# Performance work log

Hardware: AMD Instinct MI355X
Metric: run time of the kernel (lower is better)

The kernel has to match this reference:

```python
import jax, jax.numpy as jnp
import numpy as np

N_INST = 2_000_000   # total instances
D_IN = 32
D_HID = 64
D_OUT = 1
NUM_BAGS = 100_000   # ids in [0, NUM_BAGS)


def setup_inputs() -> dict:
    key = jax.random.key(0)
    k0, k1, k2, k3, k4 = jax.random.split(key, 5)
    x = jax.random.normal(k0, (N_INST, D_IN), dtype=jnp.float32)
    # sorted bag ids, every bag present (contiguous bags of equal size -> a
    # valid instance of sorted_randint over [0, NUM_BAGS))
    ids = (jnp.arange(N_INST, dtype=jnp.int32) // (N_INST // NUM_BAGS))[None, :]
    W1 = jax.random.normal(k1, (D_IN, D_HID), dtype=jnp.float32) / np.sqrt(D_IN)
    b1 = jax.random.normal(k2, (D_HID,), dtype=jnp.float32) * 0.01
    W2 = jax.random.normal(k3, (D_HID, D_OUT), dtype=jnp.float32) / np.sqrt(D_HID)
    b2 = jax.random.normal(k4, (D_OUT,), dtype=jnp.float32) * 0.01
    return {"x": x, "ids": ids, "W1": W1, "b1": b1, "W2": W2, "b2": b2}


def reference(x, ids, W1, b1, W2, b2):
    inner_ids = ids[-1]                                    # [N] bag id per instance
    h = jax.nn.relu(x @ W1 + b1)                           # prepNN: [N, D_HID]
    # fused segment mean over bags (replaces the Python loop + boolean masks)
    sums = jax.ops.segment_sum(h, inner_ids, num_segments=NUM_BAGS)          # [B, D_HID]
    counts = jax.ops.segment_sum(jnp.ones((h.shape[0],), h.dtype), inner_ids,
                                 num_segments=NUM_BAGS)                      # [B]
    pooled = sums / counts[:, None]                        # aggregation_func = mean
    out = pooled @ W2 + b2                                 # afterNN: [B, D_OUT]
    return out
```

## Files before the change

kernel.cpp:

```cpp
#include <hip/hip_runtime.h>

#define NTHREADS 256

__global__ void __launch_bounds__(NTHREADS) bag_mlp_kernel(
    const float* __restrict__ x, const int* __restrict__ ids,
    const float* __restrict__ W1, const float* __restrict__ b1,
    const float* __restrict__ W2,
    float* __restrict__ bag_sum, float* __restrict__ bag_cnt, int n)
{
  const int lane = threadIdx.x & 63;
  const long i = (long)blockIdx.x * blockDim.x + threadIdx.x;
  const bool active = i < (long)n;

  float s = 0.f;
  float cnt = 0.f;
  int id = -1;

  if (active) {
    const float4* xp = (const float4*)(x + i * 32);
    float4 xr[8];
#pragma unroll
    for (int q = 0; q < 8; ++q) xr[q] = xp[q];
    const float* xv = (const float*)xr;

    id = ids[i];
    cnt = 1.f;

    float2 h[32];
    const float2* b1v = (const float2*)b1;
#pragma unroll
    for (int j = 0; j < 32; ++j) h[j] = b1v[j];

    const float2* W1v = (const float2*)W1;
#pragma unroll
    for (int k = 0; k < 32; ++k) {
      const float xk = xv[k];
#pragma unroll
      for (int j = 0; j < 32; ++j) {
        const float2 w = W1v[k * 32 + j];
        h[j].x = fmaf(xk, w.x, h[j].x);
        h[j].y = fmaf(xk, w.y, h[j].y);
      }
    }

    const float2* W2v = (const float2*)W2;
    float acc = 0.f;
#pragma unroll
    for (int j = 0; j < 32; ++j) {
      const float2 w = W2v[j];
      acc = fmaf(fmaxf(h[j].x, 0.f), w.x, acc);
      acc = fmaf(fmaxf(h[j].y, 0.f), w.y, acc);
    }
    s = acc;
  }

#pragma unroll
  for (int d = 1; d < 64; d <<= 1) {
    float s_up = __shfl_up(s, d, 64);
    float c_up = __shfl_up(cnt, d, 64);
    int   id_up = __shfl_up(id, d, 64);
    if (lane >= d && id_up == id) { s += s_up; cnt += c_up; }
  }
  const int id_dn = __shfl_down(id, 1, 64);
  const bool run_tail = (lane == 63) || (id != id_dn);
  if (run_tail && id >= 0) {
    atomicAdd(&bag_sum[id], s);
    atomicAdd(&bag_cnt[id], cnt);
  }
}

__global__ void __launch_bounds__(256) finalize_kernel(
    const float* __restrict__ bag_sum, const float* __restrict__ bag_cnt,
    const float* __restrict__ b2, float* __restrict__ out, int nbags)
{
  const int b = blockIdx.x * blockDim.x + threadIdx.x;
  if (b < nbags) out[b] = bag_sum[b] / bag_cnt[b] + b2[0];
}

extern "C" void kernel_launch(void* const* d_in, const int* in_sizes, int n_in,
                              void* d_out, int out_size, void* d_ws, size_t ws_size,
                              hipStream_t stream)
{
  const float* x  = (const float*)d_in[0];
  const int*   ids = (const int*)d_in[1];
  const float* W1 = (const float*)d_in[2];
  const float* b1 = (const float*)d_in[3];
  const float* W2 = (const float*)d_in[4];
  const float* b2 = (const float*)d_in[5];
  float* out = (float*)d_out;

  const int n     = in_sizes[0] / 32;
  const int nbags = out_size;

  float* bag_sum = (float*)d_ws;
  float* bag_cnt = bag_sum + nbags;

  hipMemsetAsync(d_ws, 0, (size_t)2 * nbags * sizeof(float), stream);

  const int blocks = (n + NTHREADS - 1) / NTHREADS;
  bag_mlp_kernel<<<blocks, NTHREADS, 0, stream>>>(x, ids, W1, b1, W2,
                                                  bag_sum, bag_cnt, n);

  finalize_kernel<<<(nbags + 255) / 256, 256, 0, stream>>>(bag_sum, bag_cnt,
                                                           b2, out, nbags);
}
```

Measured before the change: 419.1 us.

## Compute the hidden layer with bf16x3 MFMA over persistent 16-row wave tiles

Replaces the per-thread scalar FP32 MLP with MFMA 16x16x32 bf16 instructions. It emulates FP32 precision by splitting x and W1 into high and low bf16 parts and issuing three MFMAs per output tile. Each wave works through a contiguous range of 16-instance tiles on a fixed grid, prefetching the next tile. It merges same-bag partial sums before issuing atomics and drops the count buffer, recovering bag counts in finalize by binary search over the sorted ids. This cuts FP32 FMA work and atomic traffic, but it assumes n is a multiple of 16 and adds a small precision loss from the split bf16 products.

```diff
diff --git a/kernel.cpp b/kernel.cpp
--- a/kernel.cpp
+++ b/kernel.cpp
@@ -1,106 +1,162 @@
 #include <hip/hip_runtime.h>
 
-#define NTHREADS 256
+typedef __attribute__((ext_vector_type(8))) short short8v;
+typedef __attribute__((ext_vector_type(4))) float f32x4;
 
-__global__ void __launch_bounds__(NTHREADS) bag_mlp_kernel(
+__device__ __forceinline__ unsigned short f2bf(float f) {
+  unsigned u = __builtin_bit_cast(unsigned, f);
+  unsigned r = u + 0x7FFFu + ((u >> 16) & 1u);
+  return (unsigned short)(r >> 16);
+}
+__device__ __forceinline__ float bf2f(unsigned short h) {
+  unsigned u = ((unsigned)h) << 16;
+  return __builtin_bit_cast(float, u);
+}
+
+__global__ void __launch_bounds__(256) bag_mlp_mfma(
     const float* __restrict__ x, const int* __restrict__ ids,
     const float* __restrict__ W1, const float* __restrict__ b1,
     const float* __restrict__ W2,
-    float* __restrict__ bag_sum, float* __restrict__ bag_cnt, int n)
+    float* __restrict__ bag_sum, int ntiles, int tiles_per_wave)
 {
   const int lane = threadIdx.x & 63;
-  const long i = (long)blockIdx.x * blockDim.x + threadIdx.x;
-  const bool active = i < (long)n;
+  const int lm = lane & 15;
+  const int lg = lane >> 4;
+  const int wave = blockIdx.x * (blockDim.x >> 6) + (threadIdx.x >> 6);
 
-  float s = 0.f;
-  float cnt = 0.f;
-  int id = -1;
+  const int t0 = wave * tiles_per_wave;
+  const int t1 = min(t0 + tiles_per_wave, ntiles);
+  if (t0 >= t1) return;
 
-  if (active) {
-    const float4* xp = (const float4*)(x + i * 32);
-    float4 xr[8];
+  short8v bh[4], bl[4];
 #pragma unroll
-    for (int q = 0; q < 8; ++q) xr[q] = xp[q];
-    const float* xv = (const float*)xr;
+  for (int nt = 0; nt < 4; ++nt) {
+    const int col = lm + 16 * nt;
+#pragma unroll
+    for (int e = 0; e < 8; ++e) {
+      const int k = 16 * (e >> 2) + 4 * lg + (e & 3);
+      const float f = W1[k * 64 + col];
+      const unsigned short h = f2bf(f);
+      bh[nt][e] = (short)h;
+      bl[nt][e] = (short)f2bf(f - bf2f(h));
+    }
+  }
+  float b1c[4], w2c[4];
+#pragma unroll
+  for (int nt = 0; nt < 4; ++nt) {
+    b1c[nt] = b1[lm + 16 * nt];
+    w2c[nt] = W2[lm + 16 * nt];
+  }
 
-    id = ids[i];
-    cnt = 1.f;
+  float4 va, vb; int4 iv;
+  {
+    const long base = (long)t0 * 16;
+    const float* p = x + (base + lm) * 32 + 4 * lg;
+    va = *(const float4*)p;
+    vb = *(const float4*)(p + 16);
+    if (lm == 0) iv = *(const int4*)(ids + base + 4 * lg);
+  }
 
-    float2 h[32];
-    const float2* b1v = (const float2*)b1;
-#pragma unroll
-    for (int j = 0; j < 32; ++j) h[j] = b1v[j];
-
-    const float2* W1v = (const float2*)W1;
-#pragma unroll
-    for (int k = 0; k < 32; ++k) {
-      const float xk = xv[k];
-#pragma unroll
-      for (int j = 0; j < 32; ++j) {
-        const float2 w = W1v[k * 32 + j];
-        h[j].x = fmaf(xk, w.x, h[j].x);
-        h[j].y = fmaf(xk, w.y, h[j].y);
-      }
+  for (int t = t0; t < t1; ++t) {
+    float4 nva, nvb; int4 niv;
+    if (t + 1 < t1) {
+      const long base = (long)(t + 1) * 16;
+      const float* p = x + (base + lm) * 32 + 4 * lg;
+      nva = *(const float4*)p;
+      nvb = *(const float4*)(p + 16);
+      if (lm == 0) niv = *(const int4*)(ids + base + 4 * lg);
     }
 
-    const float2* W2v = (const float2*)W2;
-    float acc = 0.f;
+    short8v ah, al;
 #pragma unroll
-    for (int j = 0; j < 32; ++j) {
-      const float2 w = W2v[j];
-      acc = fmaf(fmaxf(h[j].x, 0.f), w.x, acc);
-      acc = fmaf(fmaxf(h[j].y, 0.f), w.y, acc);
+    for (int j = 0; j < 4; ++j) {
+      const float f = ((const float*)&va)[j];
+      const unsigned short h = f2bf(f);
+      ah[j] = (short)h; al[j] = (short)f2bf(f - bf2f(h));
+      const float g = ((const float*)&vb)[j];
+      const unsigned short h2 = f2bf(g);
+      ah[4 + j] = (short)h2; al[4 + j] = (short)f2bf(g - bf2f(h2));
     }
-    s = acc;
-  }
 
+    f32x4 acc[4];
 #pragma unroll
-  for (int d = 1; d < 64; d <<= 1) {
-    float s_up = __shfl_up(s, d, 64);
-    float c_up = __shfl_up(cnt, d, 64);
-    int   id_up = __shfl_up(id, d, 64);
-    if (lane >= d && id_up == id) { s += s_up; cnt += c_up; }
-  }
-  const int id_dn = __shfl_down(id, 1, 64);
-  const bool run_tail = (lane == 63) || (id != id_dn);
-  if (run_tail && id >= 0) {
-    atomicAdd(&bag_sum[id], s);
-    atomicAdd(&bag_cnt[id], cnt);
+    for (int nt = 0; nt < 4; ++nt) {
+      f32x4 a = {0.f, 0.f, 0.f, 0.f};
+      a = __builtin_amdgcn_mfma_f32_16x16x32_bf16(ah, bh[nt], a, 0, 0, 0);
+      a = __builtin_amdgcn_mfma_f32_16x16x32_bf16(ah, bl[nt], a, 0, 0, 0);
+      a = __builtin_amdgcn_mfma_f32_16x16x32_bf16(al, bh[nt], a, 0, 0, 0);
+      acc[nt] = a;
+    }
+
+    float ps[4];
+#pragma unroll
+    for (int r = 0; r < 4; ++r) {
+      float s = 0.f;
+#pragma unroll
+      for (int nt = 0; nt < 4; ++nt) {
+        const float h = acc[nt][r] + b1c[nt];
+        s = fmaf(fmaxf(h, 0.f), w2c[nt], s);
+      }
+      ps[r] = s;
+    }
+#pragma unroll
+    for (int m = 1; m < 16; m <<= 1) {
+#pragma unroll
+      for (int r = 0; r < 4; ++r) ps[r] += __shfl_xor(ps[r], m, 64);
+    }
+
+    if (lm == 0) {
+      float a0 = ps[0], a1 = ps[1], a2 = ps[2], a3 = ps[3];
+      const int i0 = iv.x, i1 = iv.y, i2 = iv.z, i3 = iv.w;
+      if (i1 == i0) a1 += a0; else atomicAdd(&bag_sum[i0], a0);
+      if (i2 == i1) a2 += a1; else atomicAdd(&bag_sum[i1], a1);
+      if (i3 == i2) a3 += a2; else atomicAdd(&bag_sum[i2], a2);
+      atomicAdd(&bag_sum[i3], a3);
+    }
+
+    va = nva; vb = nvb; iv = niv;
   }
 }
 
 __global__ void __launch_bounds__(256) finalize_kernel(
-    const float* __restrict__ bag_sum, const float* __restrict__ bag_cnt,
-    const float* __restrict__ b2, float* __restrict__ out, int nbags)
+    const float* __restrict__ bag_sum, const int* __restrict__ ids,
+    const float* __restrict__ b2, float* __restrict__ out, int nbags, int n)
 {
   const int b = blockIdx.x * blockDim.x + threadIdx.x;
-  if (b < nbags) out[b] = bag_sum[b] / bag_cnt[b] + b2[0];
+  if (b >= nbags) return;
+  int lo0 = 0, hi0 = n;
+  while (lo0 < hi0) { const int mid = (lo0 + hi0) >> 1; if (ids[mid] < b) lo0 = mid + 1; else hi0 = mid; }
+  int lo1 = lo0, hi1 = n;
+  while (lo1 < hi1) { const int mid = (lo1 + hi1) >> 1; if (ids[mid] < b + 1) lo1 = mid + 1; else hi1 = mid; }
+  const float c = (float)(lo1 - lo0);
+  out[b] = bag_sum[b] / c + b2[0];
 }
 
 extern "C" void kernel_launch(void* const* d_in, const int* in_sizes, int n_in,
                               void* d_out, int out_size, void* d_ws, size_t ws_size,
                               hipStream_t stream)
 {
-  const float* x  = (const float*)d_in[0];
+  const float* x   = (const float*)d_in[0];
   const int*   ids = (const int*)d_in[1];
-  const float* W1 = (const float*)d_in[2];
-  const float* b1 = (const float*)d_in[3];
-  const float* W2 = (const float*)d_in[4];
-  const float* b2 = (const float*)d_in[5];
+  const float* W1  = (const float*)d_in[2];
+  const float* b1  = (const float*)d_in[3];
+  const float* W2  = (const float*)d_in[4];
+  const float* b2  = (const float*)d_in[5];
   float* out = (float*)d_out;
 
   const int n     = in_sizes[0] / 32;
   const int nbags = out_size;
 
   float* bag_sum = (float*)d_ws;
-  float* bag_cnt = bag_sum + nbags;
+  hipMemsetAsync(bag_sum, 0, (size_t)nbags * sizeof(float), stream);
 
-  hipMemsetAsync(d_ws, 0, (size_t)2 * nbags * sizeof(float), stream);
+  const int ntiles  = n / 16;
+  const int nblocks = 2048;
+  const int nwaves  = nblocks * 4;
+  const int tpw     = (ntiles + nwaves - 1) / nwaves;
 
-  const int blocks = (n + NTHREADS - 1) / NTHREADS;
-  bag_mlp_kernel<<<blocks, NTHREADS, 0, stream>>>(x, ids, W1, b1, W2,
-                                                  bag_sum, bag_cnt, n);
-
-  finalize_kernel<<<(nbags + 255) / 256, 256, 0, stream>>>(bag_sum, bag_cnt,
-                                                           b2, out, nbags);
+  bag_mlp_mfma<<<nblocks, 256, 0, stream>>>(x, ids, W1, b1, W2, bag_sum,
+                                            ntiles, tpw);
+  finalize_kernel<<<(nbags + 255) / 256, 256, 0, stream>>>(bag_sum, ids, b2,
+                                                           out, nbags, n);
 }
```

After: 372.0 us. 11.2% less time.
